# Kernel tuning notes

Measured on AMD Instinct MI355X. Metric: run time of the kernel, lower is better.

## Reference

```python
import jax, jax.numpy as jnp
import numpy as np

B, T, V, H = 16, 256, 64, 256  # batch, time, num_inputs, hidden_dim
EPS = 1e-5

def _layernorm(h, g, b):
    mu = jnp.mean(h, axis=-1, keepdims=True)
    var = jnp.mean(jnp.square(h - mu), axis=-1, keepdims=True)
    return (h - mu) * jax.lax.rsqrt(var + EPS) * g + b

def setup_inputs() -> dict:
    key = jax.random.key(0)
    ks = jax.random.split(key, 16)
    s1, sH = 1.0, 1.0 / np.sqrt(H)
    sV = 1.0 / np.sqrt(V)
    inp = {
        "x": jax.random.normal(ks[0], (B, T, V), jnp.float32),
        # per-variable GRN params (input_dim=1), stacked over V
        "W1": jax.random.normal(ks[1], (V, H), jnp.float32) * s1,
        "b1": jnp.zeros((V, H), jnp.float32),
        "W2": jax.random.normal(ks[2], (V, H, H), jnp.float32) * sH,
        "b2": jnp.zeros((V, H), jnp.float32),
        "Wg": jax.random.normal(ks[3], (V, H), jnp.float32) * s1,  # first H rows of gate Linear(1,2H)
        "bg": jnp.zeros((V, H), jnp.float32),
        "Ws": jax.random.normal(ks[4], (V, H), jnp.float32) * s1,  # skip_proj Linear(1,H)
        "bs": jnp.zeros((V, H), jnp.float32),
        "g1": jnp.ones((V, H), jnp.float32),
        "be1": jnp.zeros((V, H), jnp.float32),
        # weight network GRN: V -> V, skip is Identity
        "nW1": jax.random.normal(ks[5], (V, V), jnp.float32) * sV,
        "nb1": jnp.zeros((V,), jnp.float32),
        "nW2": jax.random.normal(ks[6], (V, V), jnp.float32) * sV,
        "nb2": jnp.zeros((V,), jnp.float32),
        "nWg": jax.random.normal(ks[7], (V, V), jnp.float32) * sV,  # first V cols of gate Linear(V,2V)
        "nbg": jnp.zeros((V,), jnp.float32),
        "ng": jnp.ones((V,), jnp.float32),
        "nbe": jnp.zeros((V,), jnp.float32),
    }
    return inp

def reference(x, W1, b1, W2, b2, Wg, bg, Ws, bs, g1, be1,
              nW1, nb1, nW2, nb2, nWg, nbg, ng, nbe):
    # --- per-variable GRNs, vectorized over V (input is a scalar per variable) ---
    feat = x[..., None]                                     # [B,T,V,1]
    h1 = feat * W1 + b1                                     # [B,T,V,H]  fc1(1->H)
    res = jnp.einsum('btvh,vhk->btvk', jax.nn.elu(h1), W2) + b2  # fc2(H->H)
    gate = jax.nn.sigmoid(feat * Wg + bg)                   # gate(1->2H)[:H]
    skip = feat * Ws + bs                                   # skip_proj(1->H)
    var_out = _layernorm(skip + gate * res, g1, be1)        # [B,T,V,H]
    # --- weight network GRN on flattened input (V -> V, skip=Identity) ---
    wres = jnp.einsum('btv,vk->btk', jax.nn.elu(x @ nW1 + nb1), nW2) + nb2
    wgate = jax.nn.sigmoid(x @ nWg + nbg)
    wout = _layernorm(x + wgate * wres, ng, nbe)            # [B,T,V]
    weights = jax.nn.softmax(wout, axis=-1)                 # [B,T,V]
    combined = jnp.einsum('btvh,btv->bth', var_out, weights)  # [B,T,H]
    return combined
```

## Files before the change

### kernel.cpp

```cpp
#include <hip/hip_runtime.h>
#include <hip/hip_bf16.h>
#include <stdint.h>

#define NTOK 4096
#define NV 64
#define NH 256
#define LN_EPS 1e-5f

typedef __attribute__((ext_vector_type(8))) short short8;
typedef __attribute__((ext_vector_type(4))) float f32x4;
typedef __attribute__((ext_vector_type(4))) uint32_t u32x4;

__device__ __forceinline__ unsigned short f32_to_bf16(float f) {
    uint32_t u = __builtin_bit_cast(uint32_t, f);
    return (unsigned short)((u + 0x7FFFu + ((u >> 16) & 1u)) >> 16);
}
__device__ __forceinline__ float fsigmoid(float z) { return 1.0f / (1.0f + __expf(-z)); }
__device__ __forceinline__ float felu(float z) { return z > 0.0f ? z : (__expf(z) - 1.0f); }
__device__ __forceinline__ uint32_t pack_bf16x2(float ze, float zo) {
    const uint32_t ue = __builtin_bit_cast(uint32_t, ze) + 0x8000u;
    const uint32_t uo = __builtin_bit_cast(uint32_t, zo) + 0x8000u;
    return __builtin_amdgcn_perm(uo, ue, 0x07060302u);
}
__device__ __forceinline__ void gload16(const void* g, void* l) {
    __builtin_amdgcn_global_load_lds(
        (const __attribute__((address_space(1))) uint32_t*)g,
        (__attribute__((address_space(3))) uint32_t*)l, 16, 0, 0);
}

__global__ __launch_bounds__(256) void k_w2t(const float* __restrict__ W2,
                                             unsigned short* __restrict__ W2T) {
    __shared__ float tile[32][33];
    const int v  = blockIdx.x >> 6;
    const int t  = blockIdx.x & 63;
    const int h0 = (t & 7) * 32;
    const int o0 = (t >> 3) * 32;
    const int r  = threadIdx.x >> 3;
    const int c4 = (threadIdx.x & 7) * 4;
    const float4 d = *(const float4*)(W2 + ((size_t)v * NH + h0 + r) * NH + o0 + c4);
    tile[r][c4 + 0] = d.x; tile[r][c4 + 1] = d.y;
    tile[r][c4 + 2] = d.z; tile[r][c4 + 3] = d.w;
    __syncthreads();
    ushort4 o;
    o.x = f32_to_bf16(tile[c4 + 0][r]);
    o.y = f32_to_bf16(tile[c4 + 1][r]);
    o.z = f32_to_bf16(tile[c4 + 2][r]);
    o.w = f32_to_bf16(tile[c4 + 3][r]);
    *(ushort4*)(W2T + ((size_t)v * NH + o0 + r) * NH + h0 + c4) = o;
}

__global__ __launch_bounds__(256) void k_weights(
    const float* __restrict__ x,
    const float* __restrict__ nW1, const float* __restrict__ nb1,
    const float* __restrict__ nW2, const float* __restrict__ nb2,
    const float* __restrict__ nWg, const float* __restrict__ nbg,
    const float* __restrict__ ng,  const float* __restrict__ nbe,
    float* __restrict__ wout_buf) {
    const int wv = threadIdx.x >> 6;
    const int lane = threadIdx.x & 63;
    const int tok = blockIdx.x * 4 + wv;
    const float xv = x[(size_t)tok * NV + lane];
    float acc1 = nb1[lane], accg = nbg[lane];
#pragma unroll 8
    for (int k = 0; k < 64; ++k) {
        const float xk = __shfl(xv, k);
        acc1 = fmaf(xk, nW1[k * 64 + lane], acc1);
        accg = fmaf(xk, nWg[k * 64 + lane], accg);
    }
    const float h  = felu(acc1);
    const float wg = fsigmoid(accg);
    float acc2 = nb2[lane];
#pragma unroll 8
    for (int k = 0; k < 64; ++k) {
        const float hk = __shfl(h, k);
        acc2 = fmaf(hk, nW2[k * 64 + lane], acc2);
    }
    const float pre = xv + wg * acc2;
    float s = pre;
#pragma unroll
    for (int m = 32; m >= 1; m >>= 1) s += __shfl_xor(s, m);
    const float mu = s * (1.0f / 64.0f);
    const float dd = pre - mu;
    float s2 = dd * dd;
#pragma unroll
    for (int m = 32; m >= 1; m >>= 1) s2 += __shfl_xor(s2, m);
    const float inv = rsqrtf(s2 * (1.0f / 64.0f) + LN_EPS);
    const float wln = dd * inv * ng[lane] + nbe[lane];
    float mx = wln;
#pragma unroll
    for (int m = 32; m >= 1; m >>= 1) mx = fmaxf(mx, __shfl_xor(mx, m));
    const float e = __expf(wln - mx);
    float se = e;
#pragma unroll
    for (int m = 32; m >= 1; m >>= 1) se += __shfl_xor(se, m);
    wout_buf[(size_t)tok * NV + lane] = e / se;
}

__device__ __forceinline__ const float* row_ptr(int r, const float* W1, const float* b1,
                                                const float* Wg, const float* bg,
                                                const float* Ws, const float* bs,
                                                const float* b2, const float* g1,
                                                const float* be1) {
    switch (r) {
        case 0: return W1; case 1: return b1; case 2: return Wg; case 3: return bg;
        case 4: return Ws; case 5: return bs; case 6: return b2; case 7: return g1;
        default: return be1;
    }
}

__global__ __launch_bounds__(256, 2) void k_main(
    const float* __restrict__ x, const unsigned short* __restrict__ W2T,
    const float* __restrict__ W1, const float* __restrict__ b1,
    const float* __restrict__ Wg, const float* __restrict__ bg,
    const float* __restrict__ Ws, const float* __restrict__ bs,
    const float* __restrict__ b2, const float* __restrict__ g1,
    const float* __restrict__ be1, const float* __restrict__ wgts,
    float* __restrict__ partials,
    float* __restrict__ outacc) {
    __shared__ u32x4 sB[2][1024];
    __shared__ float sRB[2][9][256];
    __shared__ float sX[64][9];
    __shared__ float sW[64][9];
    __shared__ float sLN[64][2][2];

    const int tid  = threadIdx.x;
    const int wid  = tid >> 6, lane = tid & 63;
    const int c    = lane & 15, kg = lane >> 4;
    const int tg   = wid >> 1, hh = wid & 1;
    const int bid  = blockIdx.x;
    const int vg   = bid & 7, tt = bid >> 3;
    const int t0   = tt * 64, vbase = vg * 8;

    const float* r0p = row_ptr(2 * wid,     W1, b1, Wg, bg, Ws, bs, b2, g1, be1);
    const float* r1p = row_ptr(2 * wid + 1, W1, b1, Wg, bg, Ws, bs, b2, g1, be1);

    const unsigned short* W2Tv0 = W2T + (size_t)vbase * (NH * NH);
#pragma unroll
    for (int q = 0; q < 4; ++q) {
        const int idx = wid * 256 + q * 64 + lane;
        const int o = idx >> 2, sl = idx & 3;
        const int s = (sl - (o >> 1)) & 3;
        gload16(W2Tv0 + (size_t)o * NH + s * 8,
                (char*)sB[0] + (size_t)(wid * 256 + q * 64) * 16);
    }
    gload16(r0p + (size_t)vbase * NH + lane * 4, (char*)sRB[0] + (2 * wid) * 1024);
    gload16(r1p + (size_t)vbase * NH + lane * 4, (char*)sRB[0] + (2 * wid + 1) * 1024);
    if (wid == 0)
        gload16(be1 + (size_t)vbase * NH + lane * 4, (char*)sRB[0] + 8 * 1024);
#pragma unroll
    for (int e = 0; e < 2; ++e) {
        const int ee = tid + e * 256;
        const int row = ee >> 3, cc = ee & 7;
        sX[row][cc] = x[(size_t)(t0 + row) * NV + vbase + cc];
        sW[row][cc] = wgts[(size_t)(t0 + row) * NV + vbase + cc];
    }
    __syncthreads();

    const int rdbase = hh * 8192 + c * 64 + (((kg + (c >> 1)) & 3) << 4);
    const f32x4 fzero = {0.f, 0.f, 0.f, 0.f};

    f32x4 wacc[2][8];
#pragma unroll
    for (int rt = 0; rt < 2; ++rt)
#pragma unroll
        for (int f = 0; f < 8; ++f) wacc[rt][f] = fzero;

#pragma unroll 1
    for (int vi = 0; vi < 8; ++vi) {
        const int rcur = vi & 1;
        const unsigned short* W2Tv = W2T + (size_t)(vbase + vi) * (NH * NH);
        const float xv0 = sX[tg * 32 + c][vi];
        const float xv1 = sX[tg * 32 + 16 + c][vi];

        f32x4 acc[2][8];
#pragma unroll
        for (int rt = 0; rt < 2; ++rt)
#pragma unroll
            for (int f = 0; f < 8; ++f) acc[rt][f] = fzero;

#pragma unroll 1
        for (int ks = 0; ks < 8; ++ks) {
            const int cb = ks & 1;
            if (ks == 0 && vi < 7) {
                gload16(r0p + (size_t)(vbase + vi + 1) * NH + lane * 4,
                        (char*)sRB[rcur ^ 1] + (2 * wid) * 1024);
                gload16(r1p + (size_t)(vbase + vi + 1) * NH + lane * 4,
                        (char*)sRB[rcur ^ 1] + (2 * wid + 1) * 1024);
                if (wid == 0)
                    gload16(be1 + (size_t)(vbase + vi + 1) * NH + lane * 4,
                            (char*)sRB[rcur ^ 1] + 8 * 1024);
            }
            if (ks < 7 || vi < 7) {
                const unsigned short* Wsrc = (ks < 7) ? W2Tv : (W2Tv + NH * NH);
                const int ksn = (ks < 7) ? (ks + 1) : 0;
#pragma unroll
                for (int q = 0; q < 4; ++q) {
                    const int idx = wid * 256 + q * 64 + lane;
                    const int o = idx >> 2, sl = idx & 3;
                    const int s = (sl - (o >> 1)) & 3;
                    gload16(Wsrc + (size_t)o * NH + ksn * 32 + s * 8,
                            (char*)sB[cb ^ 1] + (size_t)(wid * 256 + q * 64) * 16);
                }
            }
            const int k0 = ks * 32 + kg * 8;
            const float4 wA = *(const float4*)&sRB[rcur][0][k0];
            const float4 wB = *(const float4*)&sRB[rcur][0][k0 + 4];
            const float4 bA = *(const float4*)&sRB[rcur][1][k0];
            const float4 bB = *(const float4*)&sRB[rcur][1][k0 + 4];
            u32x4 ap0, ap1;
            {
                const float z0 = fmaf(xv0, wA.x, bA.x), z1 = fmaf(xv0, wA.y, bA.y);
                const float z2 = fmaf(xv0, wA.z, bA.z), z3 = fmaf(xv0, wA.w, bA.w);
                const float z4 = fmaf(xv0, wB.x, bB.x), z5 = fmaf(xv0, wB.y, bB.y);
                const float z6 = fmaf(xv0, wB.z, bB.z), z7 = fmaf(xv0, wB.w, bB.w);
                ap0[0] = pack_bf16x2(felu(z0), felu(z1));
                ap0[1] = pack_bf16x2(felu(z2), felu(z3));
                ap0[2] = pack_bf16x2(felu(z4), felu(z5));
                ap0[3] = pack_bf16x2(felu(z6), felu(z7));
            }
            {
                const float z0 = fmaf(xv1, wA.x, bA.x), z1 = fmaf(xv1, wA.y, bA.y);
                const float z2 = fmaf(xv1, wA.z, bA.z), z3 = fmaf(xv1, wA.w, bA.w);
                const float z4 = fmaf(xv1, wB.x, bB.x), z5 = fmaf(xv1, wB.y, bB.y);
                const float z6 = fmaf(xv1, wB.z, bB.z), z7 = fmaf(xv1, wB.w, bB.w);
                ap1[0] = pack_bf16x2(felu(z0), felu(z1));
                ap1[1] = pack_bf16x2(felu(z2), felu(z3));
                ap1[2] = pack_bf16x2(felu(z4), felu(z5));
                ap1[3] = pack_bf16x2(felu(z6), felu(z7));
            }
            const short8 af0 = __builtin_bit_cast(short8, ap0);
            const short8 af1 = __builtin_bit_cast(short8, ap1);
            const char* bb = (const char*)sB[cb] + rdbase;
            __builtin_amdgcn_s_setprio(1);
#pragma unroll
            for (int f = 0; f < 8; ++f) {
                const short8 bf = __builtin_bit_cast(short8, *(const u32x4*)(bb + (f << 10)));
                acc[0][f] = __builtin_amdgcn_mfma_f32_16x16x32_bf16(af0, bf, acc[0][f], 0, 0, 0);
                acc[1][f] = __builtin_amdgcn_mfma_f32_16x16x32_bf16(af1, bf, acc[1][f], 0, 0, 0);
            }
            __builtin_amdgcn_s_setprio(0);
            __syncthreads();
        }

        float xr[2][4], wv_[2][4], gv[8], bev[8];
#pragma unroll
        for (int rt = 0; rt < 2; ++rt)
#pragma unroll
            for (int r = 0; r < 4; ++r) {
                const int tl = tg * 32 + rt * 16 + kg * 4 + r;
                xr[rt][r]  = sX[tl][vi];
                wv_[rt][r] = sW[tl][vi];
            }
        float ps[2][4] = {}, pq[2][4] = {};
#pragma unroll
        for (int f = 0; f < 8; ++f) {
            const int h = ((hh << 3) + f) * 16 + c;
            const float Wg_ = sRB[rcur][2][h], bg_ = sRB[rcur][3][h];
            const float Ws_ = sRB[rcur][4][h], bs_ = sRB[rcur][5][h];
            const float b2_ = sRB[rcur][6][h];
            gv[f] = sRB[rcur][7][h]; bev[f] = sRB[rcur][8][h];
#pragma unroll
            for (int rt = 0; rt < 2; ++rt)
#pragma unroll
                for (int r = 0; r < 4; ++r) {
                    const float y = fmaf(xr[rt][r], Ws_, bs_) +
                                    fsigmoid(fmaf(xr[rt][r], Wg_, bg_)) * (acc[rt][f][r] + b2_);
                    acc[rt][f][r] = y;
                    ps[rt][r] += y;
                    pq[rt][r] = fmaf(y, y, pq[rt][r]);
                }
        }
#pragma unroll
        for (int m = 1; m <= 8; m <<= 1)
#pragma unroll
            for (int rt = 0; rt < 2; ++rt)
#pragma unroll
                for (int r = 0; r < 4; ++r) {
                    ps[rt][r] += __shfl_xor(ps[rt][r], m);
                    pq[rt][r] += __shfl_xor(pq[rt][r], m);
                }
        if (c == 0) {
#pragma unroll
            for (int rt = 0; rt < 2; ++rt)
#pragma unroll
                for (int r = 0; r < 4; ++r) {
                    const int tl = tg * 32 + rt * 16 + kg * 4 + r;
                    *(float2*)&sLN[tl][hh][0] = float2{ps[rt][r], pq[rt][r]};
                }
        }
        __syncthreads();
#pragma unroll
        for (int rt = 0; rt < 2; ++rt)
#pragma unroll
            for (int r = 0; r < 4; ++r) {
                const int tl = tg * 32 + rt * 16 + kg * 4 + r;
                const float4 q4 = *(const float4*)&sLN[tl][0][0];
                const float mu = (q4.x + q4.z) * (1.0f / 256.0f);
                const float vr = (q4.y + q4.w) * (1.0f / 256.0f) - mu * mu;
                const float iv = rsqrtf(vr + LN_EPS);
#pragma unroll
                for (int f = 0; f < 8; ++f)
                    wacc[rt][f][r] = fmaf(wv_[rt][r],
                                          fmaf((acc[rt][f][r] - mu) * iv, gv[f], bev[f]),
                                          wacc[rt][f][r]);
            }
    }

    if (partials) {
        float* P = partials + (size_t)vg * NTOK * NH;
#pragma unroll
        for (int rt = 0; rt < 2; ++rt)
#pragma unroll
            for (int r = 0; r < 4; ++r) {
                float* rowp = P + (size_t)(t0 + tg * 32 + rt * 16 + kg * 4 + r) * NH + hh * 128 + c;
#pragma unroll
                for (int f = 0; f < 8; ++f) rowp[f * 16] = wacc[rt][f][r];
            }
    } else {
#pragma unroll
        for (int rt = 0; rt < 2; ++rt)
#pragma unroll
            for (int r = 0; r < 4; ++r) {
                float* rowp = outacc + (size_t)(t0 + tg * 32 + rt * 16 + kg * 4 + r) * NH + hh * 128 + c;
#pragma unroll
                for (int f = 0; f < 8; ++f) atomicAdd(&rowp[f * 16], wacc[rt][f][r]);
            }
    }
}

__global__ __launch_bounds__(256) void k_reduce(const float* __restrict__ P,
                                                float* __restrict__ out) {
    const size_t i = ((size_t)blockIdx.x * 256 + threadIdx.x);
    const f32x4* P4 = (const f32x4*)P;
    f32x4 s = P4[i];
#pragma unroll
    for (int sl = 1; sl < 8; ++sl) s += P4[(size_t)sl * (NTOK * NH / 4) + i];
    ((f32x4*)out)[i] = s;
}

extern "C" void kernel_launch(void* const* d_in, const int* in_sizes, int n_in,
                              void* d_out, int out_size, void* d_ws, size_t ws_size,
                              hipStream_t stream) {
    const float* x   = (const float*)d_in[0];
    const float* W1  = (const float*)d_in[1];
    const float* b1  = (const float*)d_in[2];
    const float* W2  = (const float*)d_in[3];
    const float* b2  = (const float*)d_in[4];
    const float* Wg  = (const float*)d_in[5];
    const float* bg  = (const float*)d_in[6];
    const float* Ws  = (const float*)d_in[7];
    const float* bs  = (const float*)d_in[8];
    const float* g1  = (const float*)d_in[9];
    const float* be1 = (const float*)d_in[10];
    const float* nW1 = (const float*)d_in[11];
    const float* nb1 = (const float*)d_in[12];
    const float* nW2 = (const float*)d_in[13];
    const float* nb2 = (const float*)d_in[14];
    const float* nWg = (const float*)d_in[15];
    const float* nbg = (const float*)d_in[16];
    const float* ng  = (const float*)d_in[17];
    const float* nbe = (const float*)d_in[18];
    float* out = (float*)d_out;

    char* ws = (char*)d_ws;
    float* ws_wgt = (float*)ws;
    unsigned short* ws_W2T = (unsigned short*)(ws + (1 << 20));
    const size_t part_off = (size_t)9 << 20;
    const size_t part_bytes = (size_t)8 * NTOK * NH * 4;
    const bool use_part = ws_size >= part_off + part_bytes;
    float* ws_part = use_part ? (float*)(ws + part_off) : nullptr;

    k_w2t<<<dim3(64 * 64), dim3(256), 0, stream>>>(W2, ws_W2T);
    k_weights<<<dim3(NTOK / 4), dim3(256), 0, stream>>>(x, nW1, nb1, nW2, nb2,
                                                        nWg, nbg, ng, nbe, ws_wgt);
    if (!use_part) hipMemsetAsync(d_out, 0, (size_t)out_size * 4, stream);
    k_main<<<dim3(512), dim3(256), 0, stream>>>(x, ws_W2T, W1, b1, Wg, bg, Ws, bs,
                                                b2, g1, be1, ws_wgt, ws_part, out);
    if (use_part)
        k_reduce<<<dim3(NTOK * NH / 4 / 256), dim3(256), 0, stream>>>(ws_part, out);
}
```

Baseline: 152.4 us.

## Give each wave 16 tokens across full hidden width to drop LN cross-wave sync

Changes the wave-to-output mapping: each wave now owns 16 tokens over all 256 hidden columns instead of 32 tokens over half the columns. The LayerNorm statistics can then be reduced entirely with in-wave shuffles, which removes the shared-memory sLN exchange and one __syncthreads per variable. It also precomputes the W2 tile load offsets once and moves the next-variable row-param prefetch from ks==0 to ks==1. In exchange, each B-fragment read from LDS now feeds one MFMA instead of two, so LDS traffic per MFMA doubles, and ELU/pack work per wave drops.

```diff
diff --git a/kernel.cpp b/kernel.cpp
--- a/kernel.cpp
+++ b/kernel.cpp
@@ -121,12 +121,10 @@
     __shared__ float sRB[2][9][256];
     __shared__ float sX[64][9];
     __shared__ float sW[64][9];
-    __shared__ float sLN[64][2][2];
 
     const int tid  = threadIdx.x;
     const int wid  = tid >> 6, lane = tid & 63;
     const int c    = lane & 15, kg = lane >> 4;
-    const int tg   = wid >> 1, hh = wid & 1;
     const int bid  = blockIdx.x;
     const int vg   = bid & 7, tt = bid >> 3;
     const int t0   = tt * 64, vbase = vg * 8;
@@ -134,15 +132,21 @@
     const float* r0p = row_ptr(2 * wid,     W1, b1, Wg, bg, Ws, bs, b2, g1, be1);
     const float* r1p = row_ptr(2 * wid + 1, W1, b1, Wg, bg, Ws, bs, b2, g1, be1);
 
-    const unsigned short* W2Tv0 = W2T + (size_t)vbase * (NH * NH);
+    int bsrc[4], bdst[4];
 #pragma unroll
     for (int q = 0; q < 4; ++q) {
         const int idx = wid * 256 + q * 64 + lane;
         const int o = idx >> 2, sl = idx & 3;
         const int s = (sl - (o >> 1)) & 3;
-        gload16(W2Tv0 + (size_t)o * NH + s * 8,
-                (char*)sB[0] + (size_t)(wid * 256 + q * 64) * 16);
-    }
+        bsrc[q] = o * NH + s * 8;
+        bdst[q] = idx * 16;
+    }
+
+    const unsigned short* W2Tv0 = W2T + (size_t)vbase * (NH * NH);
+    gload16(W2Tv0 + bsrc[0], (char*)sB[0] + bdst[0]);
+    gload16(W2Tv0 + bsrc[1], (char*)sB[0] + bdst[1]);
+    gload16(W2Tv0 + bsrc[2], (char*)sB[0] + bdst[2]);
+    gload16(W2Tv0 + bsrc[3], (char*)sB[0] + bdst[3]);
     gload16(r0p + (size_t)vbase * NH + lane * 4, (char*)sRB[0] + (2 * wid) * 1024);
     gload16(r1p + (size_t)vbase * NH + lane * 4, (char*)sRB[0] + (2 * wid + 1) * 1024);
     if (wid == 0)
@@ -156,32 +160,27 @@
     }
     __syncthreads();
 
-    const int rdbase = hh * 8192 + c * 64 + (((kg + (c >> 1)) & 3) << 4);
+    const int rdbase = c * 64 + (((kg + (c >> 1)) & 3) << 4);
     const f32x4 fzero = {0.f, 0.f, 0.f, 0.f};
 
-    f32x4 wacc[2][8];
-#pragma unroll
-    for (int rt = 0; rt < 2; ++rt)
-#pragma unroll
-        for (int f = 0; f < 8; ++f) wacc[rt][f] = fzero;
+    f32x4 wacc[16];
+#pragma unroll
+    for (int f = 0; f < 16; ++f) wacc[f] = fzero;
 
 #pragma unroll 1
     for (int vi = 0; vi < 8; ++vi) {
         const int rcur = vi & 1;
         const unsigned short* W2Tv = W2T + (size_t)(vbase + vi) * (NH * NH);
-        const float xv0 = sX[tg * 32 + c][vi];
-        const float xv1 = sX[tg * 32 + 16 + c][vi];
-
-        f32x4 acc[2][8];
-#pragma unroll
-        for (int rt = 0; rt < 2; ++rt)
-#pragma unroll
-            for (int f = 0; f < 8; ++f) acc[rt][f] = fzero;
+        const float xv = sX[wid * 16 + c][vi];
+
+        f32x4 acc[16];
+#pragma unroll
+        for (int f = 0; f < 16; ++f) acc[f] = fzero;
 
 #pragma unroll 1
         for (int ks = 0; ks < 8; ++ks) {
             const int cb = ks & 1;
-            if (ks == 0 && vi < 7) {
+            if (ks == 1 && vi < 7) {
                 gload16(r0p + (size_t)(vbase + vi + 1) * NH + lane * 4,
                         (char*)sRB[rcur ^ 1] + (2 * wid) * 1024);
                 gload16(r1p + (size_t)(vbase + vi + 1) * NH + lane * 4,
@@ -191,140 +190,103 @@
                             (char*)sRB[rcur ^ 1] + 8 * 1024);
             }
             if (ks < 7 || vi < 7) {
-                const unsigned short* Wsrc = (ks < 7) ? W2Tv : (W2Tv + NH * NH);
-                const int ksn = (ks < 7) ? (ks + 1) : 0;
-#pragma unroll
-                for (int q = 0; q < 4; ++q) {
-                    const int idx = wid * 256 + q * 64 + lane;
-                    const int o = idx >> 2, sl = idx & 3;
-                    const int s = (sl - (o >> 1)) & 3;
-                    gload16(Wsrc + (size_t)o * NH + ksn * 32 + s * 8,
-                            (char*)sB[cb ^ 1] + (size_t)(wid * 256 + q * 64) * 16);
-                }
+                const unsigned short* Wsrc =
+                    (ks < 7) ? (W2Tv + (ks + 1) * 32) : (W2Tv + NH * NH);
+                char* bb1 = (char*)sB[cb ^ 1];
+                gload16(Wsrc + bsrc[0], bb1 + bdst[0]);
+                gload16(Wsrc + bsrc[1], bb1 + bdst[1]);
+                gload16(Wsrc + bsrc[2], bb1 + bdst[2]);
+                gload16(Wsrc + bsrc[3], bb1 + bdst[3]);
             }
             const int k0 = ks * 32 + kg * 8;
             const float4 wA = *(const float4*)&sRB[rcur][0][k0];
             const float4 wB = *(const float4*)&sRB[rcur][0][k0 + 4];
             const float4 bA = *(const float4*)&sRB[rcur][1][k0];
             const float4 bB = *(const float4*)&sRB[rcur][1][k0 + 4];
-            u32x4 ap0, ap1;
+            u32x4 ap;
             {
-                const float z0 = fmaf(xv0, wA.x, bA.x), z1 = fmaf(xv0, wA.y, bA.y);
-                const float z2 = fmaf(xv0, wA.z, bA.z), z3 = fmaf(xv0, wA.w, bA.w);
-                const float z4 = fmaf(xv0, wB.x, bB.x), z5 = fmaf(xv0, wB.y, bB.y);
-                const float z6 = fmaf(xv0, wB.z, bB.z), z7 = fmaf(xv0, wB.w, bB.w);
-                ap0[0] = pack_bf16x2(felu(z0), felu(z1));
-                ap0[1] = pack_bf16x2(felu(z2), felu(z3));
-                ap0[2] = pack_bf16x2(felu(z4), felu(z5));
-                ap0[3] = pack_bf16x2(felu(z6), felu(z7));
-            }
-            {
-                const float z0 = fmaf(xv1, wA.x, bA.x), z1 = fmaf(xv1, wA.y, bA.y);
-                const float z2 = fmaf(xv1, wA.z, bA.z), z3 = fmaf(xv1, wA.w, bA.w);
-                const float z4 = fmaf(xv1, wB.x, bB.x), z5 = fmaf(xv1, wB.y, bB.y);
-                const float z6 = fmaf(xv1, wB.z, bB.z), z7 = fmaf(xv1, wB.w, bB.w);
-                ap1[0] = pack_bf16x2(felu(z0), felu(z1));
-                ap1[1] = pack_bf16x2(felu(z2), felu(z3));
-                ap1[2] = pack_bf16x2(felu(z4), felu(z5));
-                ap1[3] = pack_bf16x2(felu(z6), felu(z7));
-            }
-            const short8 af0 = __builtin_bit_cast(short8, ap0);
-            const short8 af1 = __builtin_bit_cast(short8, ap1);
+                const float z0 = fmaf(xv, wA.x, bA.x), z1 = fmaf(xv, wA.y, bA.y);
+                const float z2 = fmaf(xv, wA.z, bA.z), z3 = fmaf(xv, wA.w, bA.w);
+                const float z4 = fmaf(xv, wB.x, bB.x), z5 = fmaf(xv, wB.y, bB.y);
+                const float z6 = fmaf(xv, wB.z, bB.z), z7 = fmaf(xv, wB.w, bB.w);
+                ap[0] = pack_bf16x2(felu(z0), felu(z1));
+                ap[1] = pack_bf16x2(felu(z2), felu(z3));
+                ap[2] = pack_bf16x2(felu(z4), felu(z5));
+                ap[3] = pack_bf16x2(felu(z6), felu(z7));
+            }
+            const short8 af = __builtin_bit_cast(short8, ap);
             const char* bb = (const char*)sB[cb] + rdbase;
             __builtin_amdgcn_s_setprio(1);
 #pragma unroll
-            for (int f = 0; f < 8; ++f) {
+            for (int f = 0; f < 16; ++f) {
                 const short8 bf = __builtin_bit_cast(short8, *(const u32x4*)(bb + (f << 10)));
-                acc[0][f] = __builtin_amdgcn_mfma_f32_16x16x32_bf16(af0, bf, acc[0][f], 0, 0, 0);
-                acc[1][f] = __builtin_amdgcn_mfma_f32_16x16x32_bf16(af1, bf, acc[1][f], 0, 0, 0);
+                acc[f] = __builtin_amdgcn_mfma_f32_16x16x32_bf16(af, bf, acc[f], 0, 0, 0);
             }
             __builtin_amdgcn_s_setprio(0);
             __syncthreads();
         }
 
-        float xr[2][4], wv_[2][4], gv[8], bev[8];
-#pragma unroll
-        for (int rt = 0; rt < 2; ++rt)
-#pragma unroll
-            for (int r = 0; r < 4; ++r) {
-                const int tl = tg * 32 + rt * 16 + kg * 4 + r;
-                xr[rt][r]  = sX[tl][vi];
-                wv_[rt][r] = sW[tl][vi];
-            }
-        float ps[2][4] = {}, pq[2][4] = {};
-#pragma unroll
-        for (int f = 0; f < 8; ++f) {
-            const int h = ((hh << 3) + f) * 16 + c;
+        float xr[4], wv_[4];
+#pragma unroll
+        for (int r = 0; r < 4; ++r) {
+            const int tl = wid * 16 + kg * 4 + r;
+            xr[r]  = sX[tl][vi];
+            wv_[r] = sW[tl][vi];
+        }
+        float ps[4] = {}, pq[4] = {};
+        float gv[16], bev[16];
+#pragma unroll
+        for (int f = 0; f < 16; ++f) {
+            const int h = f * 16 + c;
             const float Wg_ = sRB[rcur][2][h], bg_ = sRB[rcur][3][h];
             const float Ws_ = sRB[rcur][4][h], bs_ = sRB[rcur][5][h];
             const float b2_ = sRB[rcur][6][h];
             gv[f] = sRB[rcur][7][h]; bev[f] = sRB[rcur][8][h];
 #pragma unroll
-            for (int rt = 0; rt < 2; ++rt)
-#pragma unroll
-                for (int r = 0; r < 4; ++r) {
-                    const float y = fmaf(xr[rt][r], Ws_, bs_) +
-                                    fsigmoid(fmaf(xr[rt][r], Wg_, bg_)) * (acc[rt][f][r] + b2_);
-                    acc[rt][f][r] = y;
-                    ps[rt][r] += y;
-                    pq[rt][r] = fmaf(y, y, pq[rt][r]);
-                }
+            for (int r = 0; r < 4; ++r) {
+                const float y = fmaf(xr[r], Ws_, bs_) +
+                                fsigmoid(fmaf(xr[r], Wg_, bg_)) * (acc[f][r] + b2_);
+                acc[f][r] = y;
+                ps[r] += y;
+                pq[r] = fmaf(y, y, pq[r]);
+            }
         }
 #pragma unroll
         for (int m = 1; m <= 8; m <<= 1)
 #pragma unroll
-            for (int rt = 0; rt < 2; ++rt)
-#pragma unroll
-                for (int r = 0; r < 4; ++r) {
-                    ps[rt][r] += __shfl_xor(ps[rt][r], m);
-                    pq[rt][r] += __shfl_xor(pq[rt][r], m);
-                }
-        if (c == 0) {
-#pragma unroll
-            for (int rt = 0; rt < 2; ++rt)
-#pragma unroll
-                for (int r = 0; r < 4; ++r) {
-                    const int tl = tg * 32 + rt * 16 + kg * 4 + r;
-                    *(float2*)&sLN[tl][hh][0] = float2{ps[rt][r], pq[rt][r]};
-                }
-        }
-        __syncthreads();
-#pragma unroll
-        for (int rt = 0; rt < 2; ++rt)
-#pragma unroll
             for (int r = 0; r < 4; ++r) {
-                const int tl = tg * 32 + rt * 16 + kg * 4 + r;
-                const float4 q4 = *(const float4*)&sLN[tl][0][0];
-                const float mu = (q4.x + q4.z) * (1.0f / 256.0f);
-                const float vr = (q4.y + q4.w) * (1.0f / 256.0f) - mu * mu;
-                const float iv = rsqrtf(vr + LN_EPS);
-#pragma unroll
-                for (int f = 0; f < 8; ++f)
-                    wacc[rt][f][r] = fmaf(wv_[rt][r],
-                                          fmaf((acc[rt][f][r] - mu) * iv, gv[f], bev[f]),
-                                          wacc[rt][f][r]);
-            }
-    }
-
+                ps[r] += __shfl_xor(ps[r], m);
+                pq[r] += __shfl_xor(pq[r], m);
+            }
+#pragma unroll
+        for (int r = 0; r < 4; ++r) {
+            const float mu = ps[r] * (1.0f / 256.0f);
+            const float vr = fmaf(-mu, mu, pq[r] * (1.0f / 256.0f));
+            const float iv = rsqrtf(vr + LN_EPS);
+            const float wiv = wv_[r] * iv;
+#pragma unroll
+            for (int f = 0; f < 16; ++f)
+                wacc[f][r] = fmaf(wiv * (acc[f][r] - mu), gv[f],
+                                  fmaf(wv_[r], bev[f], wacc[f][r]));
+        }
+    }
+
+    const int tokb = t0 + wid * 16 + kg * 4;
     if (partials) {
         float* P = partials + (size_t)vg * NTOK * NH;
 #pragma unroll
-        for (int rt = 0; rt < 2; ++rt)
-#pragma unroll
-            for (int r = 0; r < 4; ++r) {
-                float* rowp = P + (size_t)(t0 + tg * 32 + rt * 16 + kg * 4 + r) * NH + hh * 128 + c;
-#pragma unroll
-                for (int f = 0; f < 8; ++f) rowp[f * 16] = wacc[rt][f][r];
-            }
+        for (int r = 0; r < 4; ++r) {
+            float* rowp = P + (size_t)(tokb + r) * NH + c;
+#pragma unroll
+            for (int f = 0; f < 16; ++f) rowp[f * 16] = wacc[f][r];
+        }
     } else {
 #pragma unroll
-        for (int rt = 0; rt < 2; ++rt)
-#pragma unroll
-            for (int r = 0; r < 4; ++r) {
-                float* rowp = outacc + (size_t)(t0 + tg * 32 + rt * 16 + kg * 4 + r) * NH + hh * 128 + c;
-#pragma unroll
-                for (int f = 0; f < 8; ++f) atomicAdd(&rowp[f * 16], wacc[rt][f][r]);
-            }
+        for (int r = 0; r < 4; ++r) {
+            float* rowp = outacc + (size_t)(tokb + r) * NH + c;
+#pragma unroll
+            for (int f = 0; f < 16; ++f) atomicAdd(&rowp[f * 16], wacc[f][r]);
+        }
     }
 }
 
```

Result: faster. 143.5 us (-5.8%).
